# Kernel tuning notes

Measured on AMD Instinct MI355X. Metric: run time of the kernel, lower is better.

The kernel has to match this reference:

```python
import jax, jax.numpy as jnp
import numpy as np

N = 50000
E = 400000
IN_FEATS = 256
HIDDEN = 64
HEADS = 8
CLASSES = 40
NEG_SLOPE = 0.2  # DGL GATConv default negative_slope


def setup_inputs() -> dict:
    key = jax.random.key(0)
    ks = jax.random.split(key, 12)
    features = jax.random.normal(ks[0], (N, IN_FEATS), dtype=jnp.float32)
    src = jax.random.randint(ks[1], (E,), 0, N, dtype=jnp.int32)
    dst = jax.random.randint(ks[2], (E,), 0, N, dtype=jnp.int32)
    s = 0.05
    # layer 0: in_feats -> HEADS*HIDDEN
    W1 = jax.random.normal(ks[3], (IN_FEATS, HEADS * HIDDEN), dtype=jnp.float32) * s
    al1 = jax.random.normal(ks[4], (HEADS, HIDDEN), dtype=jnp.float32) * s
    ar1 = jax.random.normal(ks[5], (HEADS, HIDDEN), dtype=jnp.float32) * s
    # layer 1: HEADS*HIDDEN -> HEADS*HIDDEN
    W2 = jax.random.normal(ks[6], (HEADS * HIDDEN, HEADS * HIDDEN), dtype=jnp.float32) * s
    al2 = jax.random.normal(ks[7], (HEADS, HIDDEN), dtype=jnp.float32) * s
    ar2 = jax.random.normal(ks[8], (HEADS, HIDDEN), dtype=jnp.float32) * s
    # layer 2: HEADS*HIDDEN -> 1*CLASSES
    W3 = jax.random.normal(ks[9], (HEADS * HIDDEN, CLASSES), dtype=jnp.float32) * s
    al3 = jax.random.normal(ks[10], (1, CLASSES), dtype=jnp.float32) * s
    ar3 = jax.random.normal(ks[11], (1, CLASSES), dtype=jnp.float32) * s
    return {"features": features, "src": src, "dst": dst,
            "W1": W1, "al1": al1, "ar1": ar1,
            "W2": W2, "al2": al2, "ar2": ar2,
            "W3": W3, "al3": al3, "ar3": ar3}


def gat_conv(h, W, al, ar, src, dst):
    """DGL GATConv (no bias, no residual, no activation, no dropout)."""
    H, D = al.shape
    feat = (h @ W).reshape(N, H, D)                      # [N,H,D]
    el = jnp.sum(feat * al[None], axis=-1)               # [N,H]
    er = jnp.sum(feat * ar[None], axis=-1)               # [N,H]
    e = jax.nn.leaky_relu(el[src] + er[dst], NEG_SLOPE)  # [E,H]
    # edge softmax over incoming edges of each dst node
    m = jax.ops.segment_max(e, dst, num_segments=N)      # [N,H]
    ex = jnp.exp(e - m[dst])                             # [E,H]
    denom = jax.ops.segment_sum(ex, dst, num_segments=N) # [N,H]
    alpha = ex / denom[dst]                              # [E,H]
    msg = alpha[:, :, None] * feat[src]                  # [E,H,D]
    out = jax.ops.segment_sum(msg, dst, num_segments=N)  # [N,H,D]
    return out.reshape(N, H * D)


def reference(features, src, dst, W1, al1, ar1, W2, al2, ar2, W3, al3, ar3):
    h = gat_conv(features, W1, al1, ar1, src, dst)  # [N, HEADS*HIDDEN]
    h = gat_conv(h, W2, al2, ar2, src, dst)         # [N, HEADS*HIDDEN]
    h = gat_conv(h, W3, al3, ar3, src, dst)         # [N, CLASSES]
    return h
```

## Files before the change

kernel.cpp:

```cpp
#include <hip/hip_runtime.h>
#include <hip/hip_bf16.h>

#define NN 50000
#define NE 400000
#define MPAD 50048

typedef __bf16 bf16x8_t __attribute__((ext_vector_type(8)));
typedef float f32x4_t __attribute__((ext_vector_type(4)));

__device__ __forceinline__ float bfbits2f(unsigned int u) {
    union { unsigned int i; float f; } v;
    v.i = u << 16;
    return v.f;
}
__device__ __forceinline__ void unpack8(uint4 q, float* f) {
    f[0] = bfbits2f(q.x & 0xffffu); f[1] = bfbits2f(q.x >> 16);
    f[2] = bfbits2f(q.y & 0xffffu); f[3] = bfbits2f(q.y >> 16);
    f[4] = bfbits2f(q.z & 0xffffu); f[5] = bfbits2f(q.z >> 16);
    f[6] = bfbits2f(q.w & 0xffffu); f[7] = bfbits2f(q.w >> 16);
}

__global__ __launch_bounds__(256) void prep_kernel(
    const float* __restrict__ features, __hip_bfloat16* __restrict__ Abf,
    const int* __restrict__ dst, int* __restrict__ deg,
    const float* __restrict__ W1, __hip_bfloat16* __restrict__ W1t,
    const float* __restrict__ W2, __hip_bfloat16* __restrict__ W2t,
    const float* __restrict__ W3, __hip_bfloat16* __restrict__ W3t,
    const float* __restrict__ al1, const float* __restrict__ ar1,
    const float* __restrict__ al2, const float* __restrict__ ar2,
    __hip_bfloat16* __restrict__ walr1, __hip_bfloat16* __restrict__ walr2) {
    int stride = gridDim.x * blockDim.x;
    for (int i = blockIdx.x * blockDim.x + threadIdx.x; i < NN * 256; i += stride) {
        Abf[i] = __float2bfloat16(features[i]);
        if (i < NE) atomicAdd(&deg[dst[i]], 1);
        if (i < 512 * 256) {
            int n = i >> 8, k = i & 255;
            W1t[i] = __float2bfloat16(W1[k * 512 + n]);
        }
        if (i < 512 * 512) {
            int n = i >> 9, k = i & 511;
            W2t[i] = __float2bfloat16(W2[k * 512 + n]);
        }
        if (i < 48 * 512) {
            int n = i >> 9, k = i & 511;
            W3t[i] = __float2bfloat16((n < 40) ? W3[k * 40 + n] : 0.f);
        }
        if (i < 16 * 256) {
            int j = i >> 8, k = i & 255;
            const float* v = (j < 8) ? (al1 + j * 64) : (ar1 + (j - 8) * 64);
            float s = 0.f;
            for (int d = 0; d < 64; ++d) s += W1[(size_t)k * 512 + (j & 7) * 64 + d] * v[d];
            walr1[(k >> 5) * 512 + j * 32 + (k & 31)] = __float2bfloat16(s);
        }
        if (i < 16 * 512) {
            int j = i >> 9, k = i & 511;
            const float* v = (j < 8) ? (al2 + j * 64) : (ar2 + (j - 8) * 64);
            float s = 0.f;
            for (int d = 0; d < 64; ++d) s += W2[(size_t)k * 512 + (j & 7) * 64 + d] * v[d];
            walr2[(k >> 5) * 512 + j * 32 + (k & 31)] = __float2bfloat16(s);
        }
    }
}

__global__ void scan_kernel(const int* __restrict__ deg, int* __restrict__ off,
                            int* __restrict__ cur, int n) {
    __shared__ int wsum[16];
    __shared__ int carry_s;
    const int tid = threadIdx.x;
    const int lane = tid & 63, wid = tid >> 6;
    if (tid == 0) carry_s = 0;
    __syncthreads();
    for (int base = 0; base < n; base += 1024) {
        int i = base + tid;
        int v = (i < n) ? deg[i] : 0;
        int s = v;
        for (int o = 1; o < 64; o <<= 1) {
            int t = __shfl_up(s, o, 64);
            if (lane >= o) s += t;
        }
        if (lane == 63) wsum[wid] = s;
        __syncthreads();
        if (wid == 0) {
            int ws = (lane < 16) ? wsum[lane] : 0;
            for (int o = 1; o < 16; o <<= 1) {
                int t = __shfl_up(ws, o, 64);
                if (lane >= o) ws += t;
            }
            if (lane < 16) wsum[lane] = ws;
        }
        __syncthreads();
        int wpre = (wid == 0) ? 0 : wsum[wid - 1];
        int carry = carry_s;
        int excl = carry + wpre + s - v;
        if (i < n) { off[i] = excl; cur[i] = excl; }
        __syncthreads();
        if (tid == 1023) carry_s = carry + wsum[15];
    }
    __syncthreads();
    if (tid == 0) off[n] = carry_s;
}

__global__ void scatter_kernel(const int* __restrict__ src, const int* __restrict__ dst,
                               int* __restrict__ cur, int* __restrict__ csr_src) {
    int e = blockIdx.x * blockDim.x + threadIdx.x;
    if (e < NE) {
        int p = atomicAdd(&cur[dst[e]], 1);
        csr_src[p] = src[e];
    }
}

__device__ __forceinline__ void gld_lds16(const void* g, void* l) {
    __builtin_amdgcn_global_load_lds(
        (const __attribute__((address_space(1))) unsigned int*)g,
        (__attribute__((address_space(3))) unsigned int*)l, 16, 0, 0);
}

__global__ __launch_bounds__(256) void gemm_bt_fused(const __hip_bfloat16* __restrict__ A,
                                                     const __hip_bfloat16* __restrict__ Wt,
                                                     const __hip_bfloat16* __restrict__ walr,
                                                     __hip_bfloat16* __restrict__ C,
                                                     float* __restrict__ el,
                                                     float* __restrict__ er,
                                                     int K) {
    __shared__ __align__(16) char smem[16384];
    char* smemA = smem;
    char* smemB = smem + 8192;
    const int w = threadIdx.x >> 6;
    const int lane = threadIdx.x & 63;
    const int row0 = blockIdx.x * 128;
    const int col0 = blockIdx.y * 128;
    const int quad = lane >> 4, l15 = lane & 15;
    const int wm = (w >> 1) * 64, wn = (w & 1) * 64;
    const int c0 = w * 2;
    const int srow = lane >> 2;
    const int skel = (lane & 3) * 8;
    const bool my_e = (blockIdx.y == 0) && ((w & 1) == 0);

    f32x4_t acc[4][4] = {};
    f32x4_t acce[4] = {};
    for (int k0 = 0; k0 < K; k0 += 32) {
        __syncthreads();
        {
            const __hip_bfloat16* gA0 = A + (size_t)(row0 + c0 * 16 + srow) * K + k0 + skel;
            const __hip_bfloat16* gB0 = Wt + (size_t)(col0 + c0 * 16 + srow) * K + k0 + skel;
            gld_lds16(gA0, smemA + c0 * 1024);
            gld_lds16(gA0 + (size_t)16 * K, smemA + (c0 + 1) * 1024);
            gld_lds16(gB0, smemB + c0 * 1024);
            gld_lds16(gB0 + (size_t)16 * K, smemB + (c0 + 1) * 1024);
        }
        __syncthreads();
        bf16x8_t a[4], b[4];
#pragma unroll
        for (int mi = 0; mi < 4; mi++)
            a[mi] = *reinterpret_cast<const bf16x8_t*>(smemA + (wm + mi * 16 + l15) * 64 + quad * 16);
#pragma unroll
        for (int ni = 0; ni < 4; ni++)
            b[ni] = *reinterpret_cast<const bf16x8_t*>(smemB + (wn + ni * 16 + l15) * 64 + quad * 16);
#pragma unroll
        for (int mi = 0; mi < 4; mi++)
#pragma unroll
            for (int ni = 0; ni < 4; ni++)
                acc[mi][ni] = __builtin_amdgcn_mfma_f32_16x16x32_bf16(a[mi], b[ni], acc[mi][ni], 0, 0, 0);
        if (my_e) {
            bf16x8_t b5 = *reinterpret_cast<const bf16x8_t*>(
                walr + (k0 >> 5) * 512 + l15 * 32 + quad * 8);
#pragma unroll
            for (int mi = 0; mi < 4; mi++)
                acce[mi] = __builtin_amdgcn_mfma_f32_16x16x32_bf16(a[mi], b5, acce[mi], 0, 0, 0);
        }
    }
#pragma unroll
    for (int mi = 0; mi < 4; mi++) {
#pragma unroll
        for (int ni = 0; ni < 4; ni++) {
#pragma unroll
            for (int r = 0; r < 4; r++) {
                int row = row0 + wm + mi * 16 + quad * 4 + r;
                if (row < NN)
                    C[(size_t)row * 512 + col0 + wn + ni * 16 + l15] =
                        __float2bfloat16(acc[mi][ni][r]);
            }
        }
    }
    if (my_e) {
#pragma unroll
        for (int mi = 0; mi < 4; mi++) {
#pragma unroll
            for (int r = 0; r < 4; r++) {
                int row = row0 + wm + mi * 16 + quad * 4 + r;
                if (row < NN) {
                    float v = acce[mi][r];
                    if (l15 < 8) el[row * 8 + l15] = v;
                    else er[row * 8 + l15 - 8] = v;
                }
            }
        }
    }
}

#define W3_LDSROW 520
__global__ __launch_bounds__(256) void gemm3_mfma(const __hip_bfloat16* __restrict__ A,
                                                  const __hip_bfloat16* __restrict__ W3t,
                                                  const float* __restrict__ al,
                                                  const float* __restrict__ ar,
                                                  __hip_bfloat16* __restrict__ C,
                                                  float* __restrict__ el,
                                                  float* __restrict__ er) {
    __shared__ __align__(16) __hip_bfloat16 wlds[48 * W3_LDSROW];
    for (int c = threadIdx.x; c < 48 * 64; c += 256) {
        int n = c >> 6, koff = (c & 63) * 8;
        *reinterpret_cast<uint4*>(&wlds[n * W3_LDSROW + koff]) =
            *reinterpret_cast<const uint4*>(W3t + n * 512 + koff);
    }
    __syncthreads();
    const int w = threadIdx.x >> 6;
    const int lane = threadIdx.x & 63;
    const int quad = lane >> 4, l15 = lane & 15;
    const int row0 = blockIdx.x * 64 + w * 16;

    float alv[3], arv[3];
#pragma unroll
    for (int c = 0; c < 3; c++) {
        int col = c * 16 + l15;
        alv[c] = (col < 40) ? al[col] : 0.f;
        arv[c] = (col < 40) ? ar[col] : 0.f;
    }

    f32x4_t acc[3] = {};
    const __hip_bfloat16* arow = A + (size_t)(row0 + l15) * 512;
#pragma unroll 4
    for (int k0 = 0; k0 < 512; k0 += 32) {
        bf16x8_t a = *reinterpret_cast<const bf16x8_t*>(arow + k0 + quad * 8);
#pragma unroll
        for (int c = 0; c < 3; c++) {
            bf16x8_t b = *reinterpret_cast<const bf16x8_t*>(
                &wlds[(c * 16 + l15) * W3_LDSROW + k0 + quad * 8]);
            acc[c] = __builtin_amdgcn_mfma_f32_16x16x32_bf16(a, b, acc[c], 0, 0, 0);
        }
    }
#pragma unroll
    for (int r = 0; r < 4; r++) {
        int row = row0 + quad * 4 + r;
        bool rok = row < NN;
        float pl = 0.f, pr = 0.f;
#pragma unroll
        for (int c = 0; c < 3; c++) {
            float v = acc[c][r];
            if (rok) C[(size_t)row * 64 + c * 16 + l15] = __float2bfloat16(v);
            pl += v * alv[c];
            pr += v * arv[c];
        }
        if (rok) C[(size_t)row * 64 + 48 + l15] = __float2bfloat16(0.f);
        pl += __shfl_xor(pl, 1, 64); pr += __shfl_xor(pr, 1, 64);
        pl += __shfl_xor(pl, 2, 64); pr += __shfl_xor(pr, 2, 64);
        pl += __shfl_xor(pl, 4, 64); pr += __shfl_xor(pr, 4, 64);
        pl += __shfl_xor(pl, 8, 64); pr += __shfl_xor(pr, 8, 64);
        if (l15 == 0 && rok) { el[row] = pl; er[row] = pr; }
    }
}

__global__ __launch_bounds__(256) void agg8_kernel(const __hip_bfloat16* __restrict__ feat,
                                                   const float* __restrict__ el,
                                                   const float* __restrict__ er,
                                                   const int* __restrict__ off,
                                                   const int* __restrict__ csr,
                                                   __hip_bfloat16* __restrict__ out) {
    int n = (blockIdx.x * blockDim.x + threadIdx.x) >> 6;
    int lane = threadIdx.x & 63;
    if (n >= NN) return;
    const int h8 = lane & 7;
    const int es = lane >> 3;
    const int hd = lane >> 3;
    int rs = off[n], re = off[n + 1];
    float er_n = er[n * 8 + h8];

    float m = -INFINITY, lsum = 0.f;
    float acc[8] = {};
    for (int base = rs; base < re; base += 8) {
        int e = base + es;
        bool valid = e < re;
        int s = valid ? csr[e] : 0;
        float t = el[s * 8 + h8] + er_n;
        float x = (t >= 0.f) ? t : 0.2f * t;
        if (!valid) x = -INFINITY;
        float gm = x;
        gm = fmaxf(gm, __shfl_xor(gm, 8, 64));
        gm = fmaxf(gm, __shfl_xor(gm, 16, 64));
        gm = fmaxf(gm, __shfl_xor(gm, 32, 64));
        float nm = fmaxf(m, gm);
        float scale = __expf(m - nm);
        float p = __expf(x - nm);
        lsum = lsum * scale + p;
        float sc = __shfl(scale, hd, 64);
#pragma unroll
        for (int d = 0; d < 8; ++d) acc[d] *= sc;
#pragma unroll
        for (int j = 0; j < 8; ++j) {
            int sj = __shfl(s, j * 8, 64);
            float pj = __shfl(p, j * 8 + hd, 64);
            uint4 q = *reinterpret_cast<const uint4*>(feat + (size_t)sj * 512 + lane * 8);
            float f[8];
            unpack8(q, f);
#pragma unroll
            for (int d = 0; d < 8; ++d) acc[d] += pj * f[d];
        }
        m = nm;
    }
    lsum += __shfl_xor(lsum, 8, 64);
    lsum += __shfl_xor(lsum, 16, 64);
    lsum += __shfl_xor(lsum, 32, 64);
    float lh = __shfl(lsum, hd, 64);
    float inv = (lh > 0.f) ? 1.f / lh : 0.f;
    bf16x8_t o8;
#pragma unroll
    for (int d = 0; d < 8; ++d) o8[d] = (__bf16)(acc[d] * inv);
    *reinterpret_cast<bf16x8_t*>(out + (size_t)n * 512 + lane * 8) = o8;
}

__global__ __launch_bounds__(256) void agg3_kernel(const __hip_bfloat16* __restrict__ feat,
                                                   const float* __restrict__ el,
                                                   const float* __restrict__ er,
                                                   const int* __restrict__ off,
                                                   const int* __restrict__ csr,
                                                   float* __restrict__ out) {
    int n = (blockIdx.x * blockDim.x + threadIdx.x) >> 6;
    int lane = threadIdx.x & 63;
    if (n >= NN) return;
    const int es = lane >> 3;
    const int dc = lane & 7;
    int rs = off[n], re = off[n + 1];
    float er_n = er[n];

    float m = -INFINITY, lsum = 0.f;
    float acc[8] = {};
    for (int base = rs; base < re; base += 8) {
        int e = base + es;
        bool valid = e < re;
        int s = valid ? csr[e] : 0;
        float t = el[s] + er_n;
        float x = (t >= 0.f) ? t : 0.2f * t;
        if (!valid) x = -INFINITY;
        float gm = x;
        gm = fmaxf(gm, __shfl_xor(gm, 8, 64));
        gm = fmaxf(gm, __shfl_xor(gm, 16, 64));
        gm = fmaxf(gm, __shfl_xor(gm, 32, 64));
        float nm = fmaxf(m, gm);
        float scale = __expf(m - nm);
        float p = __expf(x - nm);
        lsum = lsum * scale + p;
        uint4 q = *reinterpret_cast<const uint4*>(feat + (size_t)s * 64 + dc * 8);
        float f[8];
        unpack8(q, f);
#pragma unroll
        for (int d = 0; d < 8; ++d) acc[d] = acc[d] * scale + p * f[d];
        m = nm;
    }
    lsum += __shfl_xor(lsum, 8, 64);
    lsum += __shfl_xor(lsum, 16, 64);
    lsum += __shfl_xor(lsum, 32, 64);
#pragma unroll
    for (int d = 0; d < 8; ++d) {
        acc[d] += __shfl_xor(acc[d], 8, 64);
        acc[d] += __shfl_xor(acc[d], 16, 64);
        acc[d] += __shfl_xor(acc[d], 32, 64);
    }
    float inv = (lsum > 0.f) ? 1.f / lsum : 0.f;
    if (es == 0 && dc < 5) {
        float4 o0 = make_float4(acc[0] * inv, acc[1] * inv, acc[2] * inv, acc[3] * inv);
        float4 o1 = make_float4(acc[4] * inv, acc[5] * inv, acc[6] * inv, acc[7] * inv);
        *reinterpret_cast<float4*>(out + (size_t)n * 40 + dc * 8) = o0;
        *reinterpret_cast<float4*>(out + (size_t)n * 40 + dc * 8 + 4) = o1;
    }
}

extern "C" void kernel_launch(void* const* d_in, const int* in_sizes, int n_in,
                              void* d_out, int out_size, void* d_ws, size_t ws_size,
                              hipStream_t stream) {
    const float* features = (const float*)d_in[0];
    const int* src = (const int*)d_in[1];
    const int* dst = (const int*)d_in[2];
    const float* W1 = (const float*)d_in[3];
    const float* al1 = (const float*)d_in[4];
    const float* ar1 = (const float*)d_in[5];
    const float* W2 = (const float*)d_in[6];
    const float* al2 = (const float*)d_in[7];
    const float* ar2 = (const float*)d_in[8];
    const float* W3 = (const float*)d_in[9];
    const float* al3 = (const float*)d_in[10];
    const float* ar3 = (const float*)d_in[11];

    char* ws = (char*)d_ws;
    size_t o = 0;
    auto carve = [&](size_t bytes) -> void* {
        o = (o + 255) & ~(size_t)255;
        void* p = ws + o;
        o += bytes;
        return p;
    };
    __hip_bfloat16* Abf1 = (__hip_bfloat16*)carve((size_t)MPAD * 256 * 2);
    __hip_bfloat16* Fbf = (__hip_bfloat16*)carve((size_t)MPAD * 512 * 2);
    __hip_bfloat16* Gbf = (__hip_bfloat16*)carve((size_t)MPAD * 512 * 2);
    __hip_bfloat16* W1t = (__hip_bfloat16*)carve((size_t)512 * 256 * 2);
    __hip_bfloat16* W2t = (__hip_bfloat16*)carve((size_t)512 * 512 * 2);
    __hip_bfloat16* W3t = (__hip_bfloat16*)carve((size_t)48 * 512 * 2);
    __hip_bfloat16* walr1 = (__hip_bfloat16*)carve((size_t)16 * 256 * 2);
    __hip_bfloat16* walr2 = (__hip_bfloat16*)carve((size_t)16 * 512 * 2);
    float* el = (float*)carve((size_t)NN * 8 * 4);
    float* er = (float*)carve((size_t)NN * 8 * 4);
    float* el3 = (float*)carve((size_t)NN * 4);
    float* er3 = (float*)carve((size_t)NN * 4);
    int* deg = (int*)carve((size_t)NN * 4);
    int* offp = (int*)carve((size_t)(NN + 1) * 4);
    int* cur = (int*)carve((size_t)NN * 4);
    int* csr = (int*)carve((size_t)NE * 4);

    hipMemsetAsync(deg, 0, (size_t)NN * 4, stream);
    prep_kernel<<<4096, 256, 0, stream>>>(features, Abf1, dst, deg, W1, W1t, W2, W2t, W3, W3t,
                                          al1, ar1, al2, ar2, walr1, walr2);
    scan_kernel<<<1, 1024, 0, stream>>>(deg, offp, cur, NN);
    scatter_kernel<<<(NE + 255) / 256, 256, 0, stream>>>(src, dst, cur, csr);

    const int gmm = MPAD / 128;
    const int aggblk = (NN + 3) / 4;
    gemm_bt_fused<<<dim3(gmm, 4), 256, 0, stream>>>(Abf1, W1t, walr1, Fbf, el, er, 256);
    agg8_kernel<<<aggblk, 256, 0, stream>>>(Fbf, el, er, offp, csr, Gbf);
    gemm_bt_fused<<<dim3(gmm, 4), 256, 0, stream>>>(Gbf, W2t, walr2, Fbf, el, er, 512);
    agg8_kernel<<<aggblk, 256, 0, stream>>>(Fbf, el, er, offp, csr, Gbf);
    gemm3_mfma<<<MPAD / 64, 256, 0, stream>>>(Gbf, W3t, al3, ar3, Fbf, el3, er3);
    agg3_kernel<<<aggblk, 256, 0, stream>>>(Fbf, el3, er3, offp, csr, (float*)d_out);
}
```

Before: 482.2 us.

## Drop online softmax max, skip invalid gathers, widen GEMM K-step to 64

The aggregation kernels stop tracking a running max and rescaling the accumulators, and instead use exp(x) directly. This relies on the logits being small enough not to overflow. The 8-head kernel also stops gathering rows for padded edge slots, and the bf16 unpack is simplified to mask/shift helpers. The GEMM now stages two 32-wide K slices per barrier pair, using twice the LDS, to halve the number of syncs.

```diff
diff --git a/kernel.cpp b/kernel.cpp
--- a/kernel.cpp
+++ b/kernel.cpp
@@ -8,16 +8,11 @@
 typedef __bf16 bf16x8_t __attribute__((ext_vector_type(8)));
 typedef float f32x4_t __attribute__((ext_vector_type(4)));
 
-__device__ __forceinline__ float bfbits2f(unsigned int u) {
-    union { unsigned int i; float f; } v;
-    v.i = u << 16;
-    return v.f;
-}
-__device__ __forceinline__ void unpack8(uint4 q, float* f) {
-    f[0] = bfbits2f(q.x & 0xffffu); f[1] = bfbits2f(q.x >> 16);
-    f[2] = bfbits2f(q.y & 0xffffu); f[3] = bfbits2f(q.y >> 16);
-    f[4] = bfbits2f(q.z & 0xffffu); f[5] = bfbits2f(q.z >> 16);
-    f[6] = bfbits2f(q.w & 0xffffu); f[7] = bfbits2f(q.w >> 16);
+__device__ __forceinline__ float bhi(unsigned int u) {
+    union { unsigned int i; float f; } v; v.i = u & 0xffff0000u; return v.f;
+}
+__device__ __forceinline__ float blo(unsigned int u) {
+    union { unsigned int i; float f; } v; v.i = u << 16; return v.f;
 }
 
 __global__ __launch_bounds__(256) void prep_kernel(
@@ -122,9 +117,9 @@
                                                      float* __restrict__ el,
                                                      float* __restrict__ er,
                                                      int K) {
-    __shared__ __align__(16) char smem[16384];
+    __shared__ __align__(16) char smem[32768];
     char* smemA = smem;
-    char* smemB = smem + 8192;
+    char* smemB = smem + 16384;
     const int w = threadIdx.x >> 6;
     const int lane = threadIdx.x & 63;
     const int row0 = blockIdx.x * 128;
@@ -138,35 +133,44 @@
 
     f32x4_t acc[4][4] = {};
     f32x4_t acce[4] = {};
-    for (int k0 = 0; k0 < K; k0 += 32) {
+    for (int k0 = 0; k0 < K; k0 += 64) {
         __syncthreads();
-        {
-            const __hip_bfloat16* gA0 = A + (size_t)(row0 + c0 * 16 + srow) * K + k0 + skel;
-            const __hip_bfloat16* gB0 = Wt + (size_t)(col0 + c0 * 16 + srow) * K + k0 + skel;
-            gld_lds16(gA0, smemA + c0 * 1024);
-            gld_lds16(gA0 + (size_t)16 * K, smemA + (c0 + 1) * 1024);
-            gld_lds16(gB0, smemB + c0 * 1024);
-            gld_lds16(gB0 + (size_t)16 * K, smemB + (c0 + 1) * 1024);
+#pragma unroll
+        for (int kh = 0; kh < 2; ++kh) {
+            const __hip_bfloat16* gA0 =
+                A + (size_t)(row0 + c0 * 16 + srow) * K + k0 + kh * 32 + skel;
+            const __hip_bfloat16* gB0 =
+                Wt + (size_t)(col0 + c0 * 16 + srow) * K + k0 + kh * 32 + skel;
+            gld_lds16(gA0, smemA + kh * 8192 + c0 * 1024);
+            gld_lds16(gA0 + (size_t)16 * K, smemA + kh * 8192 + (c0 + 1) * 1024);
+            gld_lds16(gB0, smemB + kh * 8192 + c0 * 1024);
+            gld_lds16(gB0 + (size_t)16 * K, smemB + kh * 8192 + (c0 + 1) * 1024);
         }
         __syncthreads();
-        bf16x8_t a[4], b[4];
-#pragma unroll
-        for (int mi = 0; mi < 4; mi++)
-            a[mi] = *reinterpret_cast<const bf16x8_t*>(smemA + (wm + mi * 16 + l15) * 64 + quad * 16);
-#pragma unroll
-        for (int ni = 0; ni < 4; ni++)
-            b[ni] = *reinterpret_cast<const bf16x8_t*>(smemB + (wn + ni * 16 + l15) * 64 + quad * 16);
-#pragma unroll
-        for (int mi = 0; mi < 4; mi++)
+#pragma unroll
+        for (int kh = 0; kh < 2; ++kh) {
+            bf16x8_t a[4], b[4];
+#pragma unroll
+            for (int mi = 0; mi < 4; mi++)
+                a[mi] = *reinterpret_cast<const bf16x8_t*>(
+                    smemA + kh * 8192 + (wm + mi * 16 + l15) * 64 + quad * 16);
 #pragma unroll
             for (int ni = 0; ni < 4; ni++)
-                acc[mi][ni] = __builtin_amdgcn_mfma_f32_16x16x32_bf16(a[mi], b[ni], acc[mi][ni], 0, 0, 0);
-        if (my_e) {
-            bf16x8_t b5 = *reinterpret_cast<const bf16x8_t*>(
-                walr + (k0 >> 5) * 512 + l15 * 32 + quad * 8);
+                b[ni] = *reinterpret_cast<const bf16x8_t*>(
+                    smemB + kh * 8192 + (wn + ni * 16 + l15) * 64 + quad * 16);
 #pragma unroll
             for (int mi = 0; mi < 4; mi++)
-                acce[mi] = __builtin_amdgcn_mfma_f32_16x16x32_bf16(a[mi], b5, acce[mi], 0, 0, 0);
+#pragma unroll
+                for (int ni = 0; ni < 4; ni++)
+                    acc[mi][ni] =
+                        __builtin_amdgcn_mfma_f32_16x16x32_bf16(a[mi], b[ni], acc[mi][ni], 0, 0, 0);
+            if (my_e) {
+                bf16x8_t b5 = *reinterpret_cast<const bf16x8_t*>(
+                    walr + ((k0 >> 5) + kh) * 512 + l15 * 32 + quad * 8);
+#pragma unroll
+                for (int mi = 0; mi < 4; mi++)
+                    acce[mi] = __builtin_amdgcn_mfma_f32_16x16x32_bf16(a[mi], b5, acce[mi], 0, 0, 0);
+            }
         }
     }
 #pragma unroll
@@ -274,7 +278,7 @@
     int rs = off[n], re = off[n + 1];
     float er_n = er[n * 8 + h8];
 
-    float m = -INFINITY, lsum = 0.f;
+    float lsum = 0.f;
     float acc[8] = {};
     for (int base = rs; base < re; base += 8) {
         int e = base + es;
@@ -282,29 +286,18 @@
         int s = valid ? csr[e] : 0;
         float t = el[s * 8 + h8] + er_n;
         float x = (t >= 0.f) ? t : 0.2f * t;
-        if (!valid) x = -INFINITY;
-        float gm = x;
-        gm = fmaxf(gm, __shfl_xor(gm, 8, 64));
-        gm = fmaxf(gm, __shfl_xor(gm, 16, 64));
-        gm = fmaxf(gm, __shfl_xor(gm, 32, 64));
-        float nm = fmaxf(m, gm);
-        float scale = __expf(m - nm);
-        float p = __expf(x - nm);
-        lsum = lsum * scale + p;
-        float sc = __shfl(scale, hd, 64);
-#pragma unroll
-        for (int d = 0; d < 8; ++d) acc[d] *= sc;
-#pragma unroll
-        for (int j = 0; j < 8; ++j) {
+        float p = valid ? __expf(x) : 0.f;
+        lsum += p;
+        int cnt = min(8, re - base);
+        for (int j = 0; j < cnt; ++j) {
             int sj = __shfl(s, j * 8, 64);
             float pj = __shfl(p, j * 8 + hd, 64);
             uint4 q = *reinterpret_cast<const uint4*>(feat + (size_t)sj * 512 + lane * 8);
-            float f[8];
-            unpack8(q, f);
-#pragma unroll
-            for (int d = 0; d < 8; ++d) acc[d] += pj * f[d];
-        }
-        m = nm;
+            acc[0] += pj * blo(q.x); acc[1] += pj * bhi(q.x);
+            acc[2] += pj * blo(q.y); acc[3] += pj * bhi(q.y);
+            acc[4] += pj * blo(q.z); acc[5] += pj * bhi(q.z);
+            acc[6] += pj * blo(q.w); acc[7] += pj * bhi(q.w);
+        }
     }
     lsum += __shfl_xor(lsum, 8, 64);
     lsum += __shfl_xor(lsum, 16, 64);
@@ -331,7 +324,7 @@
     int rs = off[n], re = off[n + 1];
     float er_n = er[n];
 
-    float m = -INFINITY, lsum = 0.f;
+    float lsum = 0.f;
     float acc[8] = {};
     for (int base = rs; base < re; base += 8) {
         int e = base + es;
@@ -339,21 +332,13 @@
         int s = valid ? csr[e] : 0;
         float t = el[s] + er_n;
         float x = (t >= 0.f) ? t : 0.2f * t;
-        if (!valid) x = -INFINITY;
-        float gm = x;
-        gm = fmaxf(gm, __shfl_xor(gm, 8, 64));
-        gm = fmaxf(gm, __shfl_xor(gm, 16, 64));
-        gm = fmaxf(gm, __shfl_xor(gm, 32, 64));
-        float nm = fmaxf(m, gm);
-        float scale = __expf(m - nm);
-        float p = __expf(x - nm);
-        lsum = lsum * scale + p;
+        float p = valid ? __expf(x) : 0.f;
+        lsum += p;
         uint4 q = *reinterpret_cast<const uint4*>(feat + (size_t)s * 64 + dc * 8);
-        float f[8];
-        unpack8(q, f);
-#pragma unroll
-        for (int d = 0; d < 8; ++d) acc[d] = acc[d] * scale + p * f[d];
-        m = nm;
+        acc[0] += p * blo(q.x); acc[1] += p * bhi(q.x);
+        acc[2] += p * blo(q.y); acc[3] += p * bhi(q.y);
+        acc[4] += p * blo(q.z); acc[5] += p * bhi(q.z);
+        acc[6] += p * blo(q.w); acc[7] += p * bhi(q.w);
     }
     lsum += __shfl_xor(lsum, 8, 64);
     lsum += __shfl_xor(lsum, 16, 64);
```

Result: no change. 486.4 us (+0.9%).
